# Kernel tuning notes

Hardware: AMD Instinct MI355X
Metric: run time of the kernel (lower is better)

The kernel has to match this reference:

```python
import jax, jax.numpy as jnp
import numpy as np

B, C, H, W = 16, 4, 512, 512
ALPHA, BETA, GAMMA = 1.0, 0.7, 2.0
UPPER, LOWER = 1000.0, 200.0
W_UPPER, W_LOWER = 2.5, 20.0
SMOOTH = 1.0


def setup_inputs() -> dict:
    key = jax.random.key(0)
    k1, k2, k3 = jax.random.split(key, 3)
    outputs = jax.random.normal(k1, (B, C, H, W), dtype=jnp.float32)
    class_weight = jax.random.uniform(k2, (C,), dtype=jnp.float32, minval=0.5, maxval=2.0)
    targets = jax.random.randint(k3, (B, H, W), 0, C, dtype=jnp.int32)
    return {"outputs": outputs, "class_weight": class_weight, "targets": targets}


def _cc_dynamic_weights(tgt):
    """4-connected components of (tgt==2), then per-region area-based weight.

    tgt: [H, W] int32. Returns [H, W] float32 dynamic weight (1.0 off-mask).
    Equivalent to scipy.ndimage.label (default 4-connectivity) + per-region
    piecewise-linear weight, done GPU-side via min-label propagation with
    pointer jumping.
    """
    BIG = H * W  # sentinel label for background
    mask = tgt == 2
    idx = jnp.arange(BIG, dtype=jnp.int32).reshape(H, W)
    lbl0 = jnp.where(mask, idx, BIG)

    def cond(state):
        prev, cur = state
        return jnp.any(prev != cur)

    def body(state):
        _, lbl = state
        p = jnp.pad(lbl, 1, constant_values=BIG)
        nmin = jnp.minimum(jnp.minimum(p[:-2, 1:-1], p[2:, 1:-1]),
                           jnp.minimum(p[1:-1, :-2], p[1:-1, 2:]))
        new = jnp.where(mask, jnp.minimum(lbl, nmin), BIG)
        # pointer jumping: label <- label of my current label's pixel
        new = jnp.where(mask, new.reshape(-1)[new], BIG)  # OOB gather clipped, then masked
        return (lbl, new)

    _, lbl = jax.lax.while_loop(cond, body, (jnp.full_like(lbl0, -1), lbl0))

    # region area per pixel via scatter-add on root labels (background -> bin BIG)
    counts = jnp.zeros(BIG + 1, jnp.float32).at[lbl.reshape(-1)].add(
        mask.reshape(-1).astype(jnp.float32))
    area = counts[lbl]  # [H, W]

    interp = W_UPPER + (W_LOWER - W_UPPER) * (UPPER - area) / (UPPER - LOWER)
    rw = jnp.where(area > UPPER, W_UPPER, jnp.where(area < LOWER, W_LOWER, interp))
    return jnp.where(mask, rw, 1.0).astype(jnp.float32)


def reference(outputs, class_weight, targets):
    nc = outputs.shape[1]
    # weighted per-pixel cross entropy (reduction='none')
    logp = jax.nn.log_softmax(outputs, axis=1)  # [B,C,H,W]
    nll = -jnp.take_along_axis(logp, targets[:, None, :, :], axis=1)[:, 0]  # [B,H,W]
    ce = class_weight[targets] * nll  # [B,H,W]

    dyn = jax.vmap(_cc_dynamic_weights)(targets)  # [B,H,W]
    weighted_ce = jnp.mean(ce * dyn)

    probs = jax.nn.softmax(outputs, axis=1)
    one_hot = jax.nn.one_hot(targets, nc, dtype=jnp.float32).transpose(0, 3, 1, 2)
    inter = jnp.sum(probs * one_hot, axis=(2, 3))  # [B,C]
    dice = (2.0 * inter + SMOOTH) / (jnp.sum(probs, axis=(2, 3)) + jnp.sum(one_hot, axis=(2, 3)) + SMOOTH)
    dice_loss = 1.0 - jnp.mean(dice)

    pt = jnp.exp(-ce)
    focal = jnp.mean(ALPHA * (1.0 - pt) ** GAMMA * ce)

    return BETA * weighted_ce + (1.0 - BETA) * dice_loss + focal
```

## Files before the change

kernel.cpp:

```cpp
#include <hip/hip_runtime.h>


namespace {
constexpr int IMG_W = 512;
constexpr int NB    = 16;
constexpr int NC    = 4;
constexpr int HW    = 512 * 512;
constexpr int NPIX  = NB * HW;
constexpr int SLAB  = 4096;
constexpr int NSLAB = NPIX / SLAB;
constexpr int NID   = NPIX / 2;
constexpr int LOSS_BLOCKS = 2048;
constexpr int PART_STRIDE = 16;
constexpr float ALPHA  = 1.0f;
constexpr float BETA   = 0.7f;
constexpr float UPPER  = 1000.0f;
constexpr float LOWER  = 200.0f;
constexpr float W_UP   = 2.5f;
constexpr float W_LO   = 20.0f;
constexpr float SMOOTH = 1.0f;
}

__device__ __forceinline__ int ld_par(const int* parent, int i) {
    return __hip_atomic_load(&parent[i], __ATOMIC_RELAXED, __HIP_MEMORY_SCOPE_AGENT);
}

__device__ __forceinline__ int find_root_g(int* parent, int x) {
    int p = ld_par(parent, x);
    while (p != x) { x = p; p = ld_par(parent, x); }
    return x;
}

__device__ __forceinline__ void unite_g(int* parent, int a, int b) {
    int ra = find_root_g(parent, a);
    int rb = find_root_g(parent, b);
    while (ra != rb) {
        int lo = ra < rb ? ra : rb;
        int hi = ra < rb ? rb : ra;
        int old = atomicCAS(&parent[hi], hi, lo);
        if (old == hi) return;
        ra = find_root_g(parent, old);
        rb = find_root_g(parent, lo);
    }
}

__device__ __forceinline__ int ld_lp(int* lp, int i) {
    return __hip_atomic_load(&lp[i], __ATOMIC_RELAXED, __HIP_MEMORY_SCOPE_WORKGROUP);
}

__device__ __forceinline__ int find_l(int* lp, int x) {
    int p = ld_lp(lp, x);
    while (p != x) { x = p; p = ld_lp(lp, x); }
    return x;
}

__device__ __forceinline__ void unite_l(int* lp, int a, int b) {
    int ra = find_l(lp, a);
    int rb = find_l(lp, b);
    while (ra != rb) {
        int lo = ra < rb ? ra : rb;
        int hi = ra < rb ? rb : ra;
        int old = atomicCAS(&lp[hi], hi, lo);
        if (old == hi) return;
        ra = find_l(lp, old);
        rb = find_l(lp, lo);
    }
}

__device__ __forceinline__ float wave_reduce(float v) {
    #pragma unroll
    for (int off = 32; off > 0; off >>= 1) v += __shfl_down(v, off);
    return v;
}

__global__ void __launch_bounds__(256)
k1_init(const int* __restrict__ tgt, int* __restrict__ parent,
        int* __restrict__ counts) {
    __shared__ int lp[SLAB];
    const int tid = threadIdx.x, bid = blockIdx.x;
    const int base = bid * SLAB;
    const int lane = tid & 63;

    unsigned mk16 = 0;
    #pragma unroll
    for (int it = 0; it < 16; ++it) {
        int l = it * 256 + tid;
        bool mk = (tgt[base + l] == 2);
        mk16 |= (unsigned)mk << it;
        unsigned long long bal = __ballot(mk);
        int par = -1;
        if (mk) {
            unsigned long long below = (1ull << lane) - 1ull;
            unsigned long long zb = (~bal) & below;
            int rs = (zb == 0ull) ? 0 : (64 - __clzll(zb));
            par = l - lane + rs;
        }
        lp[l] = par;
    }
    {
        int c0 = bid * (NID / NSLAB) + tid * 8;
        *reinterpret_cast<int4*>(&counts[c0])     = make_int4(0, 0, 0, 0);
        *reinterpret_cast<int4*>(&counts[c0 + 4]) = make_int4(0, 0, 0, 0);
    }
    __syncthreads();

    #pragma unroll 1
    for (int it = 0; it < 16; ++it) {
        if (!((mk16 >> it) & 1u)) continue;
        int l = it * 256 + tid;
        if (lane == 0 && (l & (IMG_W - 1)) != 0 && ld_lp(lp, l - 1) >= 0)
            unite_l(lp, l, l - 1);
        if (it >= 2 && ((mk16 >> (it - 2)) & 1u))
            unite_l(lp, l, l - IMG_W);
    }
    __syncthreads();

    #pragma unroll
    for (int q = 0; q < 4; ++q) {
        int l0 = (q * 256 + tid) * 4;
        int vj[4];
        #pragma unroll
        for (int j = 0; j < 4; ++j) {
            int l = l0 + j;
            int p = lp[l];
            if (p < 0) { vj[j] = -1; continue; }
            while (true) { int n = lp[p]; if (n == p) break; p = n; }
            vj[j] = base + p;
        }
        *reinterpret_cast<int4*>(&parent[base + l0]) =
            make_int4(vj[0], vj[1], vj[2], vj[3]);
    }
}

__global__ void __launch_bounds__(256)
k2_boundary(const int* __restrict__ tgt, int* parent) {
    int gid = blockIdx.x * 256 + threadIdx.x;
    int s   = gid >> 9;
    int col = gid & 511;
    if ((s & 63) == 0) return;
    int px = s * SLAB + col;
    if (tgt[px] == 2 && tgt[px - IMG_W] == 2) unite_g(parent, px, px - IMG_W);
}

__global__ void __launch_bounds__(256)
k3_flatten(int* parent, int* counts) {
    int q0 = (blockIdx.x * 256 + threadIdx.x) * 4;
    int4 pv = *reinterpret_cast<const int4*>(&parent[q0]);
    int vj[4] = {pv.x, pv.y, pv.z, pv.w};
    bool any = false;
    #pragma unroll
    for (int j = 0; j < 4; ++j) {
        int v = vj[j];
        if (v == -1) continue;
        int id;
        while (true) {
            if (v <= -2) { id = -2 - v; break; }
            int nxt = ld_par(parent, v);
            if (nxt == v)  { id = v >> 1; break; }
            if (nxt <= -2) { id = -2 - nxt; break; }
            v = nxt;
        }
        vj[j] = -2 - id;
        any = true;
        atomicAdd(&counts[id], 1);
    }
    if (any)
        *reinterpret_cast<int4*>(&parent[q0]) = make_int4(vj[0], vj[1], vj[2], vj[3]);
}

__global__ void __launch_bounds__(256)
k4_loss(const float* __restrict__ logits, const float* __restrict__ cw,
        const int* __restrict__ tgt, const int* __restrict__ parent,
        const int* __restrict__ counts, float* __restrict__ partials) {
    const int bid = blockIdx.x, tid = threadIdx.x;
    const int b    = bid >> 7;
    const int slab = bid & 127;
    const float* Lb = logits + (size_t)b * NC * HW;
    const int*   Tb = tgt + (size_t)b * HW;
    const int*   Pb = parent + (size_t)b * HW;
    float cw0 = cw[0], cw1 = cw[1], cw2 = cw[2], cw3 = cw[3];

    float a_wce = 0.f, a_foc = 0.f;
    float a_ps[4] = {0.f, 0.f, 0.f, 0.f};
    float a_in[4] = {0.f, 0.f, 0.f, 0.f};
    float a_ct[4] = {0.f, 0.f, 0.f, 0.f};

    #pragma unroll
    for (int it = 0; it < 2; ++it) {
        int p = slab * 2048 + (it * 256 + tid) * 4;
        int4 t4 = *reinterpret_cast<const int4*>(&Tb[p]);
        int4 e4 = *reinterpret_cast<const int4*>(&Pb[p]);
        int tj[4] = {t4.x, t4.y, t4.z, t4.w};
        int ej[4] = {e4.x, e4.y, e4.z, e4.w};
        float4 x0 = *reinterpret_cast<const float4*>(&Lb[p]);
        float4 x1 = *reinterpret_cast<const float4*>(&Lb[p + HW]);
        float4 x2 = *reinterpret_cast<const float4*>(&Lb[p + 2 * HW]);
        float4 x3 = *reinterpret_cast<const float4*>(&Lb[p + 3 * HW]);
        float c0[4] = {x0.x, x0.y, x0.z, x0.w};
        float c1[4] = {x1.x, x1.y, x1.z, x1.w};
        float c2[4] = {x2.x, x2.y, x2.z, x2.w};
        float c3[4] = {x3.x, x3.y, x3.z, x3.w};
        #pragma unroll
        for (int j = 0; j < 4; ++j) {
            float v0 = c0[j], v1 = c1[j], v2 = c2[j], v3 = c3[j];
            int   t  = tj[j];
            float m  = fmaxf(fmaxf(v0, v1), fmaxf(v2, v3));
            float e0 = __expf(v0 - m), e1 = __expf(v1 - m);
            float e2 = __expf(v2 - m), e3 = __expf(v3 - m);
            float S  = e0 + e1 + e2 + e3;
            float invS = __frcp_rn(S);
            float xt = (t == 0) ? v0 : (t == 1) ? v1 : (t == 2) ? v2 : v3;
            float wt = (t == 0) ? cw0 : (t == 1) ? cw1 : (t == 2) ? cw2 : cw3;
            float nll = __logf(S) + m - xt;
            float ce  = wt * nll;
            float pt  = __expf(-ce);
            float omp = 1.0f - pt;
            float focal_i = ALPHA * omp * omp * ce;
            float dyn = 1.0f;
            if (t == 2) {
                float area = (float)counts[-2 - ej[j]];
                float interp = W_UP + (W_LO - W_UP) * (UPPER - area) * (1.0f / (UPPER - LOWER));
                dyn = (area > UPPER) ? W_UP : (area < LOWER) ? W_LO : interp;
            }
            float pr0 = e0 * invS, pr1 = e1 * invS, pr2 = e2 * invS, pr3 = e3 * invS;
            float prt = (t == 0) ? pr0 : (t == 1) ? pr1 : (t == 2) ? pr2 : pr3;
            a_wce += ce * dyn;
            a_foc += focal_i;
            a_ps[0] += pr0; a_ps[1] += pr1; a_ps[2] += pr2; a_ps[3] += pr3;
            a_in[t] += prt;
            a_ct[t] += 1.0f;
        }
    }

    float vals[14];
    vals[0] = a_wce; vals[1] = a_foc;
    vals[2] = a_ps[0]; vals[3] = a_ps[1]; vals[4] = a_ps[2]; vals[5] = a_ps[3];
    vals[6] = a_in[0]; vals[7] = a_in[1]; vals[8] = a_in[2]; vals[9] = a_in[3];
    vals[10] = a_ct[0]; vals[11] = a_ct[1]; vals[12] = a_ct[2]; vals[13] = a_ct[3];

    __shared__ float red[14][4];
    int lane = tid & 63, wv = tid >> 6;
    #pragma unroll
    for (int i = 0; i < 14; ++i) {
        float v = wave_reduce(vals[i]);
        if (lane == 0) red[i][wv] = v;
    }
    __syncthreads();
    if (tid < 14)
        partials[bid * PART_STRIDE + tid] =
            red[tid][0] + red[tid][1] + red[tid][2] + red[tid][3];
}

__global__ void __launch_bounds__(1024)
k5_final(const float* __restrict__ partials, float* __restrict__ out) {
    int tid = threadIdx.x, lane = tid & 63, w = tid >> 6;
    const float* r0 = &partials[(w * 128 + lane) * PART_STRIDE];
    const float* r1 = &partials[(w * 128 + 64 + lane) * PART_STRIDE];
    float v[14];
    #pragma unroll
    for (int i = 0; i < 14; ++i) v[i] = r0[i] + r1[i];
    #pragma unroll
    for (int i = 0; i < 14; ++i) v[i] = wave_reduce(v[i]);

    __shared__ double s_wce[16], s_foc[16], s_dice[16];
    if (lane == 0) {
        double dsum = 0.0;
        #pragma unroll
        for (int c = 0; c < 4; ++c) {
            double inter = v[6 + c], psum = v[2 + c], cnt = v[10 + c];
            dsum += (2.0 * inter + (double)SMOOTH) / (psum + cnt + (double)SMOOTH);
        }
        s_wce[w] = v[0]; s_foc[w] = v[1]; s_dice[w] = dsum;
    }
    __syncthreads();
    if (tid == 0) {
        double wce = 0.0, foc = 0.0, dice = 0.0;
        for (int i = 0; i < 16; ++i) { wce += s_wce[i]; foc += s_foc[i]; dice += s_dice[i]; }
        double dice_mean = dice / (double)(NB * NC);
        out[0] = (float)((double)BETA * (wce / (double)NPIX)
                         + (1.0 - (double)BETA) * (1.0 - dice_mean)
                         + (foc / (double)NPIX));
    }
}

extern "C" void kernel_launch(void* const* d_in, const int* in_sizes, int n_in,
                              void* d_out, int out_size, void* d_ws, size_t ws_size,
                              hipStream_t stream) {
    const float* logits = (const float*)d_in[0];
    const float* cw     = (const float*)d_in[1];
    const int*   tgt    = (const int*)d_in[2];
    float*       out    = (float*)d_out;
    char*        ws     = (char*)d_ws;
    int*   parent   = (int*)ws;
    int*   counts   = (int*)(ws + (size_t)NPIX * 4);
    float* partials = (float*)(ws + (size_t)NPIX * 4 + (size_t)NID * 4);

    hipLaunchKernelGGL(k1_init, dim3(NSLAB), dim3(256), 0, stream,
                       tgt, parent, counts);
    hipLaunchKernelGGL(k2_boundary, dim3(NSLAB * IMG_W / 256), dim3(256), 0, stream,
                       tgt, parent);
    hipLaunchKernelGGL(k3_flatten, dim3(NPIX / 1024), dim3(256), 0, stream,
                       parent, counts);
    hipLaunchKernelGGL(k4_loss, dim3(LOSS_BLOCKS), dim3(256), 0, stream,
                       logits, cw, tgt, parent, counts, partials);
    hipLaunchKernelGGL(k5_final, dim3(1), dim3(1024), 0, stream, partials, out);
}
```

Before: 183.5 us.

## Count slab-local component areas in shared memory and fuse final reduction into loss kernel

The init kernel now computes component areas in shared memory. It flags components touching open slab boundaries and writes final counts directly for fully interior components, so only boundary-touching components go through the global flatten and atomic-count pass. The parent array also encodes the target class for non-mask pixels, which lets the loss kernel drop its separate target read. The final reduction kernel is removed in favour of a last-block-done pattern with an atomic counter. This cuts global atomics, memory traffic and one launch, but adds more shared-memory passes in the init kernel and relies on correct release/acquire ordering.

```diff
diff --git a/kernel.cpp b/kernel.cpp
--- a/kernel.cpp
+++ b/kernel.cpp
@@ -48,22 +48,17 @@
     return __hip_atomic_load(&lp[i], __ATOMIC_RELAXED, __HIP_MEMORY_SCOPE_WORKGROUP);
 }
 
-__device__ __forceinline__ int find_l(int* lp, int x) {
-    int p = ld_lp(lp, x);
-    while (p != x) { x = p; p = ld_lp(lp, x); }
-    return x;
-}
-
 __device__ __forceinline__ void unite_l(int* lp, int a, int b) {
-    int ra = find_l(lp, a);
-    int rb = find_l(lp, b);
+    int ra = a, rb = b;
+    { int p = ld_lp(lp, ra); while (p != ra) { ra = p; p = ld_lp(lp, ra); } }
+    { int p = ld_lp(lp, rb); while (p != rb) { rb = p; p = ld_lp(lp, rb); } }
     while (ra != rb) {
         int lo = ra < rb ? ra : rb;
         int hi = ra < rb ? rb : ra;
         int old = atomicCAS(&lp[hi], hi, lo);
         if (old == hi) return;
-        ra = find_l(lp, old);
-        rb = find_l(lp, lo);
+        { int p = old; while (true) { int n = ld_lp(lp, p); if (n == p) break; p = n; } ra = p; }
+        { int p = lo;  while (true) { int n = ld_lp(lp, p); if (n == p) break; p = n; } rb = p; }
     }
 }
 
@@ -75,32 +70,34 @@
 
 __global__ void __launch_bounds__(256)
 k1_init(const int* __restrict__ tgt, int* __restrict__ parent,
-        int* __restrict__ counts) {
+        int* __restrict__ counts, int* __restrict__ done) {
     __shared__ int lp[SLAB];
+    __shared__ int larea[SLAB];
     const int tid = threadIdx.x, bid = blockIdx.x;
     const int base = bid * SLAB;
     const int lane = tid & 63;
+    if (bid == 0 && tid == 0)
+        __hip_atomic_store(done, 0, __ATOMIC_RELAXED, __HIP_MEMORY_SCOPE_AGENT);
 
     unsigned mk16 = 0;
     #pragma unroll
     for (int it = 0; it < 16; ++it) {
         int l = it * 256 + tid;
-        bool mk = (tgt[base + l] == 2);
+        int t = tgt[base + l];
+        bool mk = (t == 2);
         mk16 |= (unsigned)mk << it;
         unsigned long long bal = __ballot(mk);
-        int par = -1;
+        int par;
         if (mk) {
             unsigned long long below = (1ull << lane) - 1ull;
             unsigned long long zb = (~bal) & below;
             int rs = (zb == 0ull) ? 0 : (64 - __clzll(zb));
             par = l - lane + rs;
+        } else {
+            par = -(1 + t);
         }
         lp[l] = par;
-    }
-    {
-        int c0 = bid * (NID / NSLAB) + tid * 8;
-        *reinterpret_cast<int4*>(&counts[c0])     = make_int4(0, 0, 0, 0);
-        *reinterpret_cast<int4*>(&counts[c0 + 4]) = make_int4(0, 0, 0, 0);
+        larea[l] = 0;
     }
     __syncthreads();
 
@@ -115,6 +112,20 @@
     }
     __syncthreads();
 
+    const bool top_open = (bid & 63) != 0;
+    const bool bot_open = (bid & 63) != 63;
+    #pragma unroll 1
+    for (int it = 0; it < 16; ++it) {
+        if (!((mk16 >> it) & 1u)) continue;
+        int l = it * 256 + tid;
+        int p = lp[l];
+        while (true) { int n = lp[p]; if (n == p) break; p = n; }
+        atomicAdd(&larea[p], 1);
+        if ((it < 2 && top_open) || (it >= 14 && bot_open))
+            atomicOr(&larea[p], (int)0x80000000);
+    }
+    __syncthreads();
+
     #pragma unroll
     for (int q = 0; q < 4; ++q) {
         int l0 = (q * 256 + tid) * 4;
@@ -123,9 +134,17 @@
         for (int j = 0; j < 4; ++j) {
             int l = l0 + j;
             int p = lp[l];
-            if (p < 0) { vj[j] = -1; continue; }
+            if (p < 0) { vj[j] = p; continue; }
             while (true) { int n = lp[p]; if (n == p) break; p = n; }
-            vj[j] = base + p;
+            int a = larea[p];
+            if (a < 0) {
+                vj[j] = base + p;
+                if (l == p) counts[(base + p) >> 1] = 0;
+            } else {
+                int id = (base + p) >> 1;
+                vj[j] = -8 - id;
+                if (l == p) counts[id] = a;
+            }
         }
         *reinterpret_cast<int4*>(&parent[base + l0]) =
             make_int4(vj[0], vj[1], vj[2], vj[3]);
@@ -143,7 +162,7 @@
 }
 
 __global__ void __launch_bounds__(256)
-k3_flatten(int* parent, int* counts) {
+k3_open(int* parent, int* counts) {
     int q0 = (blockIdx.x * 256 + threadIdx.x) * 4;
     int4 pv = *reinterpret_cast<const int4*>(&parent[q0]);
     int vj[4] = {pv.x, pv.y, pv.z, pv.w};
@@ -151,16 +170,15 @@
     #pragma unroll
     for (int j = 0; j < 4; ++j) {
         int v = vj[j];
-        if (v == -1) continue;
+        if (v < 0) continue;
         int id;
         while (true) {
-            if (v <= -2) { id = -2 - v; break; }
             int nxt = ld_par(parent, v);
-            if (nxt == v)  { id = v >> 1; break; }
-            if (nxt <= -2) { id = -2 - nxt; break; }
+            if (nxt == v)   { id = v >> 1;   break; }
+            if (nxt <= -8)  { id = -8 - nxt; break; }
             v = nxt;
         }
-        vj[j] = -2 - id;
+        vj[j] = -8 - id;
         any = true;
         atomicAdd(&counts[id], 1);
     }
@@ -170,13 +188,13 @@
 
 __global__ void __launch_bounds__(256)
 k4_loss(const float* __restrict__ logits, const float* __restrict__ cw,
-        const int* __restrict__ tgt, const int* __restrict__ parent,
-        const int* __restrict__ counts, float* __restrict__ partials) {
+        const int* __restrict__ parent, const int* __restrict__ counts,
+        float* __restrict__ partials, int* __restrict__ done,
+        float* __restrict__ out) {
     const int bid = blockIdx.x, tid = threadIdx.x;
     const int b    = bid >> 7;
     const int slab = bid & 127;
     const float* Lb = logits + (size_t)b * NC * HW;
-    const int*   Tb = tgt + (size_t)b * HW;
     const int*   Pb = parent + (size_t)b * HW;
     float cw0 = cw[0], cw1 = cw[1], cw2 = cw[2], cw3 = cw[3];
 
@@ -188,9 +206,7 @@
     #pragma unroll
     for (int it = 0; it < 2; ++it) {
         int p = slab * 2048 + (it * 256 + tid) * 4;
-        int4 t4 = *reinterpret_cast<const int4*>(&Tb[p]);
         int4 e4 = *reinterpret_cast<const int4*>(&Pb[p]);
-        int tj[4] = {t4.x, t4.y, t4.z, t4.w};
         int ej[4] = {e4.x, e4.y, e4.z, e4.w};
         float4 x0 = *reinterpret_cast<const float4*>(&Lb[p]);
         float4 x1 = *reinterpret_cast<const float4*>(&Lb[p + HW]);
@@ -203,7 +219,8 @@
         #pragma unroll
         for (int j = 0; j < 4; ++j) {
             float v0 = c0[j], v1 = c1[j], v2 = c2[j], v3 = c3[j];
-            int   t  = tj[j];
+            int   e  = ej[j];
+            int   t  = (e >= -4) ? (-1 - e) : 2;
             float m  = fmaxf(fmaxf(v0, v1), fmaxf(v2, v3));
             float e0 = __expf(v0 - m), e1 = __expf(v1 - m);
             float e2 = __expf(v2 - m), e3 = __expf(v3 - m);
@@ -217,8 +234,8 @@
             float omp = 1.0f - pt;
             float focal_i = ALPHA * omp * omp * ce;
             float dyn = 1.0f;
-            if (t == 2) {
-                float area = (float)counts[-2 - ej[j]];
+            if (e <= -8) {
+                float area = (float)counts[-8 - e];
                 float interp = W_UP + (W_LO - W_UP) * (UPPER - area) * (1.0f / (UPPER - LOWER));
                 dyn = (area > UPPER) ? W_UP : (area < LOWER) ? W_LO : interp;
             }
@@ -246,36 +263,51 @@
         if (lane == 0) red[i][wv] = v;
     }
     __syncthreads();
-    if (tid < 14)
-        partials[bid * PART_STRIDE + tid] =
-            red[tid][0] + red[tid][1] + red[tid][2] + red[tid][3];
-}
-
-__global__ void __launch_bounds__(1024)
-k5_final(const float* __restrict__ partials, float* __restrict__ out) {
-    int tid = threadIdx.x, lane = tid & 63, w = tid >> 6;
-    const float* r0 = &partials[(w * 128 + lane) * PART_STRIDE];
-    const float* r1 = &partials[(w * 128 + 64 + lane) * PART_STRIDE];
-    float v[14];
-    #pragma unroll
-    for (int i = 0; i < 14; ++i) v[i] = r0[i] + r1[i];
-    #pragma unroll
-    for (int i = 0; i < 14; ++i) v[i] = wave_reduce(v[i]);
-
-    __shared__ double s_wce[16], s_foc[16], s_dice[16];
-    if (lane == 0) {
-        double dsum = 0.0;
-        #pragma unroll
-        for (int c = 0; c < 4; ++c) {
-            double inter = v[6 + c], psum = v[2 + c], cnt = v[10 + c];
-            dsum += (2.0 * inter + (double)SMOOTH) / (psum + cnt + (double)SMOOTH);
-        }
-        s_wce[w] = v[0]; s_foc[w] = v[1]; s_dice[w] = dsum;
-    }
+    if (tid < 14) {
+        float s = red[tid][0] + red[tid][1] + red[tid][2] + red[tid][3];
+        __hip_atomic_store(&partials[bid * PART_STRIDE + tid], s,
+                           __ATOMIC_RELEASE, __HIP_MEMORY_SCOPE_AGENT);
+    }
+    __syncthreads();
+
+    __shared__ int lastv;
+    if (tid == 0) {
+        int prev = __hip_atomic_fetch_add(done, 1, __ATOMIC_ACQ_REL,
+                                          __HIP_MEMORY_SCOPE_AGENT);
+        lastv = (prev == LOSS_BLOCKS - 1) ? 1 : 0;
+    }
+    __syncthreads();
+    if (!lastv) return;
+
+    __shared__ double sw[4], sf[4], sd[4];
+    double dw = 0.0, df = 0.0, dd = 0.0;
+    for (int img = wv; img < NB; img += 4) {
+        float v[14];
+        #pragma unroll
+        for (int i = 0; i < 14; ++i) {
+            float a = __hip_atomic_load(&partials[(img * 128 + lane) * PART_STRIDE + i],
+                                        __ATOMIC_RELAXED, __HIP_MEMORY_SCOPE_AGENT);
+            float c = __hip_atomic_load(&partials[(img * 128 + 64 + lane) * PART_STRIDE + i],
+                                        __ATOMIC_RELAXED, __HIP_MEMORY_SCOPE_AGENT);
+            v[i] = a + c;
+        }
+        #pragma unroll
+        for (int i = 0; i < 14; ++i) v[i] = wave_reduce(v[i]);
+        if (lane == 0) {
+            dw += v[0]; df += v[1];
+            #pragma unroll
+            for (int c = 0; c < 4; ++c) {
+                double inter = v[6 + c], psum = v[2 + c], cnt = v[10 + c];
+                dd += (2.0 * inter + (double)SMOOTH) / (psum + cnt + (double)SMOOTH);
+            }
+        }
+    }
+    if (lane == 0) { sw[wv] = dw; sf[wv] = df; sd[wv] = dd; }
     __syncthreads();
     if (tid == 0) {
         double wce = 0.0, foc = 0.0, dice = 0.0;
-        for (int i = 0; i < 16; ++i) { wce += s_wce[i]; foc += s_foc[i]; dice += s_dice[i]; }
+        #pragma unroll
+        for (int i = 0; i < 4; ++i) { wce += sw[i]; foc += sf[i]; dice += sd[i]; }
         double dice_mean = dice / (double)(NB * NC);
         out[0] = (float)((double)BETA * (wce / (double)NPIX)
                          + (1.0 - (double)BETA) * (1.0 - dice_mean)
@@ -294,14 +326,15 @@
     int*   parent   = (int*)ws;
     int*   counts   = (int*)(ws + (size_t)NPIX * 4);
     float* partials = (float*)(ws + (size_t)NPIX * 4 + (size_t)NID * 4);
+    int*   done     = (int*)(ws + (size_t)NPIX * 4 + (size_t)NID * 4
+                             + (size_t)LOSS_BLOCKS * PART_STRIDE * 4);
 
     hipLaunchKernelGGL(k1_init, dim3(NSLAB), dim3(256), 0, stream,
-                       tgt, parent, counts);
+                       tgt, parent, counts, done);
     hipLaunchKernelGGL(k2_boundary, dim3(NSLAB * IMG_W / 256), dim3(256), 0, stream,
                        tgt, parent);
-    hipLaunchKernelGGL(k3_flatten, dim3(NPIX / 1024), dim3(256), 0, stream,
+    hipLaunchKernelGGL(k3_open, dim3(NPIX / 1024), dim3(256), 0, stream,
                        parent, counts);
     hipLaunchKernelGGL(k4_loss, dim3(LOSS_BLOCKS), dim3(256), 0, stream,
-                       logits, cw, tgt, parent, counts, partials);
-    hipLaunchKernelGGL(k5_final, dim3(1), dim3(1024), 0, stream, partials, out);
-}
+                       logits, cw, parent, counts, partials, done, out);
+}
```

Result: slower. 223.9 us (+22.0%).
